# Kernel optimization log

Hardware: AMD Instinct MI355X
Metric: run time of the kernel (lower is better)

The kernel has to match this reference:

```python
import jax, jax.numpy as jnp
import numpy as np

N, E, IN_DIM, HID, OUT = 50000, 800000, 128, 64, 64


def setup_inputs() -> dict:
    key = jax.random.key(0)
    ks = jax.random.split(key, 8)
    x = jax.random.normal(ks[0], (N, IN_DIM), dtype=jnp.float32)
    edge_index = jax.random.randint(ks[1], (2, E), 0, N, dtype=jnp.int64)
    # Glorot-style init like PyG GCNConv linear; bias zeros-init equivalent -> small randn for generality
    def glorot(k, fan_in, fan_out):
        s = (6.0 / (fan_in + fan_out)) ** 0.5
        return jax.random.uniform(k, (fan_in, fan_out), jnp.float32, -s, s)
    W1 = glorot(ks[2], IN_DIM, HID)
    b1 = jnp.zeros((HID,), jnp.float32)
    W2 = glorot(ks[3], HID, HID)
    b2 = jnp.zeros((HID,), jnp.float32)
    W3 = glorot(ks[4], HID, OUT)
    b3 = jnpp = jnp.zeros((OUT,), jnp.float32)
    return {"x": x, "edge_index": edge_index, "W1": W1, "b1": b1,
            "W2": W2, "b2": b2, "W3": W3, "b3": b3}


def _gcn_norm(edge_index, num_nodes):
    # PyG gcn_norm with add_self_loops=True, edge_weight=1:
    # A_hat = A + I; deg over target column; norm = d^-1/2[src] * d^-1/2[dst]
    loops = jnp.arange(num_nodes, dtype=edge_index.dtype)
    src = jnp.concatenate([edge_index[0], loops])
    dst = jnp.concatenate([edge_index[1], loops])
    ones = jnp.ones(src.shape[0], dtype=jnp.float32)
    deg = jax.ops.segment_sum(ones, dst, num_segments=num_nodes)
    dinv = jnp.where(deg > 0, jax.lax.rsqrt(deg), 0.0)
    norm = dinv[src] * dinv[dst]  # [E+N]
    return src, dst, norm


def _conv(h, src, dst, norm, W, b, num_nodes):
    h = h @ W                         # [N, F_out] dense transform first (PyG order)
    msg = norm[:, None] * h[src]      # gather + degree-normalize, [E+N, F_out]
    out = jax.ops.segment_sum(msg, dst, num_segments=num_nodes)  # scatter-add
    return out + b


def reference(x, edge_index, W1, b1, W2, b2, W3, b3):
    num_nodes = x.shape[0]
    src, dst, norm = _gcn_norm(edge_index, num_nodes)
    h = _conv(x, src, dst, norm, W1, b1, num_nodes)
    h = jax.nn.relu(h)  # dropout is identity in eval / p=0
    h = _conv(h, src, dst, norm, W2, b2, num_nodes)
    h = jax.nn.relu(h)
    h = _conv(h, src, dst, norm, W3, b3, num_nodes)
    return h
```

## Files before the change

kernel.cpp:

```cpp
#include <hip/hip_runtime.h>


#define FD 64
#define P1CHUNK 4096

typedef unsigned short ushort_t;
typedef unsigned int uint_t;

__device__ __forceinline__ ushort_t f2bf(float f) {
    uint_t u = __float_as_uint(f);
    u = (u + 0x7fffu + ((u >> 16) & 1u)) >> 16;
    return (ushort_t)u;
}
__device__ __forceinline__ uint_t pack2bf(float f0, float f1) {
    return (uint_t)f2bf(f0) | ((uint_t)f2bf(f1) << 16);
}

__global__ __launch_bounds__(256) void bucket_count(const int* __restrict__ dst,
                                                    int* __restrict__ bucketCnt, int E) {
    __shared__ int hist[256];
    int tid = threadIdx.x;
    hist[tid] = 0;
    __syncthreads();
    int base = blockIdx.x * P1CHUNK;
#pragma unroll
    for (int k = 0; k < 16; ++k) {
        int e = base + k * 256 + tid;
        if (e < E) atomicAdd(&hist[dst[e] >> 8], 1);
    }
    __syncthreads();
    int h = hist[tid];
    if (h) atomicAdd(&bucketCnt[tid], h);
}

__global__ __launch_bounds__(256) void scan_buckets(const int* __restrict__ bucketCnt,
                                                    int* __restrict__ bucketBase,
                                                    int* __restrict__ bucketCursor,
                                                    int* __restrict__ rowptr,
                                                    int NB, int N, int E) {
    __shared__ int wsum[4];
    int tid = threadIdx.x, lane = tid & 63, wv = tid >> 6;
    int v = (tid < NB) ? bucketCnt[tid] : 0;
    int x = v;
    for (int off = 1; off < 64; off <<= 1) {
        int t = __shfl_up(x, off, 64);
        if (lane >= off) x += t;
    }
    if (lane == 63) wsum[wv] = x;
    __syncthreads();
    int wex = 0;
    for (int i = 0; i < wv; ++i) wex += wsum[i];
    int excl = wex + x - v;
    if (tid < NB) { bucketBase[tid] = excl; bucketCursor[tid] = excl; }
    if (tid == 0) { bucketBase[NB] = E; rowptr[N] = E; }
}

__global__ __launch_bounds__(256) void bin_scatter(const int* __restrict__ src,
                                                   const int* __restrict__ dst,
                                                   int* __restrict__ bucketCursor,
                                                   uint_t* __restrict__ staged, int E) {
    __shared__ int hist[256];
    __shared__ int gbase[256];
    int tid = threadIdx.x;
    hist[tid] = 0;
    __syncthreads();
    int base = blockIdx.x * P1CHUNK;
#pragma unroll
    for (int k = 0; k < 16; ++k) {
        int e = base + k * 256 + tid;
        if (e < E) atomicAdd(&hist[dst[e] >> 8], 1);
    }
    __syncthreads();
    int h = hist[tid];
    gbase[tid] = h ? atomicAdd(&bucketCursor[tid], h) : 0;
    hist[tid] = 0;
    __syncthreads();
#pragma unroll
    for (int k = 0; k < 16; ++k) {
        int e = base + k * 256 + tid;
        if (e < E) {
            int s = src[e], d = dst[e];
            int b = d >> 8;
            int r = atomicAdd(&hist[b], 1);
            staged[gbase[b] + r] = (uint_t)s | ((uint_t)(d & 255) << 16);
        }
    }
}

__global__ __launch_bounds__(256) void bucket_sort(const uint_t* __restrict__ staged,
                                                   const int* __restrict__ bucketBase,
                                                   int* __restrict__ rowptr,
                                                   float* __restrict__ dinv,
                                                   ushort_t* __restrict__ csr, int N) {
    __shared__ int ncnt[256];
    __shared__ int nrp[256];
    __shared__ int wsum[4];
    int tid = threadIdx.x, lane = tid & 63, wv = tid >> 6;
    int b = blockIdx.x;
    int gbeg = bucketBase[b], gend = bucketBase[b + 1];
    int cntE = gend - gbeg;
    ncnt[tid] = 0;
    __syncthreads();
    for (int i = tid; i < cntE; i += 256)
        atomicAdd(&ncnt[(staged[gbeg + i] >> 16) & 255], 1);
    __syncthreads();
    int v = ncnt[tid];
    int x = v;
    for (int off = 1; off < 64; off <<= 1) {
        int t = __shfl_up(x, off, 64);
        if (lane >= off) x += t;
    }
    if (lane == 63) wsum[wv] = x;
    __syncthreads();
    int wex = 0;
    for (int i = 0; i < wv; ++i) wex += wsum[i];
    int excl = wex + x - v;
    nrp[tid] = excl;
    int node = b * 256 + tid;
    if (node < N) dinv[node] = rsqrtf((float)(v + 1));
    if (node <= N) rowptr[node] = gbeg + excl;
    ncnt[tid] = 0;
    __syncthreads();
    for (int i = tid; i < cntE; i += 256) {
        uint_t p = staged[gbeg + i];
        int dl = (p >> 16) & 255;
        int lofs = atomicAdd(&ncnt[dl], 1);
        csr[(size_t)gbeg + nrp[dl] + lofs] = (ushort_t)(p & 0xffffu);
    }
}

template <int K>
__global__ __launch_bounds__(256) void gemm_kernel(const float* __restrict__ x,
                                                   const float* __restrict__ W,
                                                   const float* __restrict__ dinv,
                                                   ushort_t* __restrict__ out, int nrows) {
    constexpr int KP = K + 4;
    constexpr int NC = K / 4;
    constexpr int YP = 68;
    __shared__ float Xs[64 * KP];
    const int tid = threadIdx.x;
    const int lane = tid & 63;
    const int rowBase = blockIdx.x * 64;

    for (int idx = tid; idx < 64 * NC; idx += 256) {
        int row = idx / NC, kc = idx % NC;
        int r = rowBase + row;
        float4 v = (r < nrows) ? *(const float4*)(x + (size_t)r * K + kc * 4)
                               : make_float4(0.f, 0.f, 0.f, 0.f);
        *(float4*)(&Xs[row * KP + kc * 4]) = v;
    }
    __syncthreads();

    const int c0 = __builtin_amdgcn_readfirstlane((tid >> 6) * 16);
    float acc[16];
#pragma unroll
    for (int i = 0; i < 16; ++i) acc[i] = 0.f;
    const float* Xrow = &Xs[lane * KP];

#pragma unroll 4
    for (int k = 0; k < K; k += 4) {
        float4 xv = *(const float4*)(Xrow + k);
        const float* wp = W + (size_t)k * FD + c0;
#pragma unroll
        for (int ci = 0; ci < 16; ++ci) {
            acc[ci] = fmaf(xv.x, wp[ci], acc[ci]);
            acc[ci] = fmaf(xv.y, wp[FD + ci], acc[ci]);
            acc[ci] = fmaf(xv.z, wp[2 * FD + ci], acc[ci]);
            acc[ci] = fmaf(xv.w, wp[3 * FD + ci], acc[ci]);
        }
    }

    int r = rowBase + lane;
    float di = (r < nrows) ? dinv[r] : 0.f;
    __syncthreads();
    float* Ys = Xs;
#pragma unroll
    for (int ci = 0; ci < 16; ++ci) Ys[lane * YP + c0 + ci] = acc[ci] * di;
    __syncthreads();

    for (int i = tid; i < 64 * 16; i += 256) {
        int row = i >> 4, seg = i & 15;
        int rr = rowBase + row;
        if (rr < nrows) {
            float4 v = *(const float4*)(&Ys[row * YP + seg * 4]);
            uint2 p;
            p.x = pack2bf(v.x, v.y);
            p.y = pack2bf(v.z, v.w);
            *(uint2*)(out + (size_t)rr * FD + seg * 4) = p;
        }
    }
}

__device__ __forceinline__ void bf8_acc(uint4 a, float* acc) {
    acc[0] += __uint_as_float(a.x << 16);
    acc[1] += __uint_as_float(a.x & 0xffff0000u);
    acc[2] += __uint_as_float(a.y << 16);
    acc[3] += __uint_as_float(a.y & 0xffff0000u);
    acc[4] += __uint_as_float(a.z << 16);
    acc[5] += __uint_as_float(a.z & 0xffff0000u);
    acc[6] += __uint_as_float(a.w << 16);
    acc[7] += __uint_as_float(a.w & 0xffff0000u);
}

template <bool RELU>
__global__ __launch_bounds__(256) void agg_fused(
    const int* __restrict__ rowptr, const ushort_t* __restrict__ csr,
    const float* __restrict__ dinv, const ushort_t* __restrict__ h,
    const float* __restrict__ b, float* __restrict__ out, int N) {
    int wid = (blockIdx.x * blockDim.x + threadIdx.x) >> 6;
    int lane = threadIdx.x & 63;
    int l8 = lane & 7;
    int node = wid * 8 + (lane >> 3);
    bool valid = node < N;
    int nd = valid ? node : N - 1;
    int beg = rowptr[nd];
    int end = valid ? rowptr[nd + 1] : beg;
    const uint4* __restrict__ h4 = (const uint4*)h;
    float acc[8];
#pragma unroll
    for (int k = 0; k < 8; ++k) acc[k] = 0.f;
    bf8_acc(h4[(size_t)nd * 8 + l8], acc);
    int j = beg;
    for (; j + 3 < end; j += 4) {
        int s0 = csr[j], s1 = csr[j + 1], s2 = csr[j + 2], s3 = csr[j + 3];
        uint4 a0 = h4[(size_t)s0 * 8 + l8];
        uint4 a1 = h4[(size_t)s1 * 8 + l8];
        uint4 a2 = h4[(size_t)s2 * 8 + l8];
        uint4 a3 = h4[(size_t)s3 * 8 + l8];
        bf8_acc(a0, acc); bf8_acc(a1, acc); bf8_acc(a2, acc); bf8_acc(a3, acc);
    }
    for (; j < end; ++j) bf8_acc(h4[(size_t)csr[j] * 8 + l8], acc);

    float di = dinv[nd];
    float4 b0 = *(const float4*)(b + l8 * 8);
    float4 b1 = *(const float4*)(b + l8 * 8 + 4);
    float4 v0, v1;
    v0.x = fmaf(di, acc[0], b0.x); v0.y = fmaf(di, acc[1], b0.y);
    v0.z = fmaf(di, acc[2], b0.z); v0.w = fmaf(di, acc[3], b0.w);
    v1.x = fmaf(di, acc[4], b1.x); v1.y = fmaf(di, acc[5], b1.y);
    v1.z = fmaf(di, acc[6], b1.z); v1.w = fmaf(di, acc[7], b1.w);
    if (RELU) {
        v0.x = fmaxf(v0.x, 0.f); v0.y = fmaxf(v0.y, 0.f);
        v0.z = fmaxf(v0.z, 0.f); v0.w = fmaxf(v0.w, 0.f);
        v1.x = fmaxf(v1.x, 0.f); v1.y = fmaxf(v1.y, 0.f);
        v1.z = fmaxf(v1.z, 0.f); v1.w = fmaxf(v1.w, 0.f);
    }
    if (valid) {
        float* op = out + (size_t)node * FD + l8 * 8;
        *(float4*)op = v0;
        *(float4*)(op + 4) = v1;
    }
}

extern "C" void kernel_launch(void* const* d_in, const int* in_sizes, int n_in,
                              void* d_out, int out_size, void* d_ws, size_t ws_size,
                              hipStream_t stream) {
    const float* x  = (const float*)d_in[0];
    const int*   ei = (const int*)d_in[1];
    const float* W1 = (const float*)d_in[2];
    const float* b1 = (const float*)d_in[3];
    const float* W2 = (const float*)d_in[4];
    const float* b2 = (const float*)d_in[5];
    const float* W3 = (const float*)d_in[6];
    const float* b3 = (const float*)d_in[7];
    float* out = (float*)d_out;

    const int N = in_sizes[0] / 128;
    const int E = in_sizes[1] / 2;
    const int* src = ei;
    const int* dst = ei + E;
    const int NB = (N + 255) / 256;

    float*    f1     = (float*)d_ws;
    ushort_t* hB     = (ushort_t*)(f1 + (size_t)N * FD);
    float*    dinv   = (float*)(hB + (size_t)N * FD);
    int*      rowptr = (int*)(dinv + N);
    int*   bucketCnt    = rowptr + N + 1;
    int*   bucketBase   = bucketCnt + NB;
    int*   bucketCursor = bucketBase + NB + 1;
    uint_t*   staged = (uint_t*)(bucketCursor + NB);
    ushort_t* csr    = (ushort_t*)(staged + E);

    const int nEBlk = (E + P1CHUNK - 1) / P1CHUNK;
    dim3 blk(256);
    dim3 gGemm((N + 63) / 64);
    dim3 gAgg((N + 31) / 32);

    hipMemsetAsync(bucketCnt, 0, (size_t)NB * sizeof(int), stream);
    bucket_count<<<dim3(nEBlk), blk, 0, stream>>>(dst, bucketCnt, E);
    scan_buckets<<<dim3(1), blk, 0, stream>>>(bucketCnt, bucketBase, bucketCursor,
                                              rowptr, NB, N, E);
    bin_scatter<<<dim3(nEBlk), blk, 0, stream>>>(src, dst, bucketCursor, staged, E);
    bucket_sort<<<dim3(NB), blk, 0, stream>>>(staged, bucketBase, rowptr, dinv, csr, N);

    gemm_kernel<128><<<gGemm, blk, 0, stream>>>(x, W1, dinv, hB, N);
    agg_fused<true><<<gAgg, blk, 0, stream>>>(rowptr, csr, dinv, hB, b1, f1, N);

    gemm_kernel<64><<<gGemm, blk, 0, stream>>>(f1, W2, dinv, hB, N);
    agg_fused<true><<<gAgg, blk, 0, stream>>>(rowptr, csr, dinv, hB, b2, f1, N);

    gemm_kernel<64><<<gGemm, blk, 0, stream>>>(f1, W3, dinv, hB, N);
    agg_fused<false><<<gAgg, blk, 0, stream>>>(rowptr, csr, dinv, hB, b3, out, N);
}
```

Measured before the change: 147.7 us.

## Fuse first GEMM with edge bin scatter and defer dinv scaling to bucket sort

The layer-1 GEMM no longer depends on dinv, so it is merged into the same launch as the edge bin-scatter, with block ranges split between the two jobs. Both run concurrently and one launch is saved. The dinv row scaling of the GEMM output moves into bucket_sort, which now re-reads and rewrites hB in bf16. That adds a second bf16 rounding and an extra read-modify-write pass over hB. The combined kernel also uses the larger GEMM shared-memory footprint for the scatter blocks, which may lower their occupancy.

Result: faster. 143.1 us (-3.1%).

```diff
diff --git a/kernel.cpp b/kernel.cpp
--- a/kernel.cpp
+++ b/kernel.cpp
@@ -55,92 +55,18 @@
     if (tid == 0) { bucketBase[NB] = E; rowptr[N] = E; }
 }
 
-__global__ __launch_bounds__(256) void bin_scatter(const int* __restrict__ src,
-                                                   const int* __restrict__ dst,
-                                                   int* __restrict__ bucketCursor,
-                                                   uint_t* __restrict__ staged, int E) {
-    __shared__ int hist[256];
-    __shared__ int gbase[256];
-    int tid = threadIdx.x;
-    hist[tid] = 0;
-    __syncthreads();
-    int base = blockIdx.x * P1CHUNK;
-#pragma unroll
-    for (int k = 0; k < 16; ++k) {
-        int e = base + k * 256 + tid;
-        if (e < E) atomicAdd(&hist[dst[e] >> 8], 1);
-    }
-    __syncthreads();
-    int h = hist[tid];
-    gbase[tid] = h ? atomicAdd(&bucketCursor[tid], h) : 0;
-    hist[tid] = 0;
-    __syncthreads();
-#pragma unroll
-    for (int k = 0; k < 16; ++k) {
-        int e = base + k * 256 + tid;
-        if (e < E) {
-            int s = src[e], d = dst[e];
-            int b = d >> 8;
-            int r = atomicAdd(&hist[b], 1);
-            staged[gbase[b] + r] = (uint_t)s | ((uint_t)(d & 255) << 16);
-        }
-    }
-}
-
-__global__ __launch_bounds__(256) void bucket_sort(const uint_t* __restrict__ staged,
-                                                   const int* __restrict__ bucketBase,
-                                                   int* __restrict__ rowptr,
-                                                   float* __restrict__ dinv,
-                                                   ushort_t* __restrict__ csr, int N) {
-    __shared__ int ncnt[256];
-    __shared__ int nrp[256];
-    __shared__ int wsum[4];
-    int tid = threadIdx.x, lane = tid & 63, wv = tid >> 6;
-    int b = blockIdx.x;
-    int gbeg = bucketBase[b], gend = bucketBase[b + 1];
-    int cntE = gend - gbeg;
-    ncnt[tid] = 0;
-    __syncthreads();
-    for (int i = tid; i < cntE; i += 256)
-        atomicAdd(&ncnt[(staged[gbeg + i] >> 16) & 255], 1);
-    __syncthreads();
-    int v = ncnt[tid];
-    int x = v;
-    for (int off = 1; off < 64; off <<= 1) {
-        int t = __shfl_up(x, off, 64);
-        if (lane >= off) x += t;
-    }
-    if (lane == 63) wsum[wv] = x;
-    __syncthreads();
-    int wex = 0;
-    for (int i = 0; i < wv; ++i) wex += wsum[i];
-    int excl = wex + x - v;
-    nrp[tid] = excl;
-    int node = b * 256 + tid;
-    if (node < N) dinv[node] = rsqrtf((float)(v + 1));
-    if (node <= N) rowptr[node] = gbeg + excl;
-    ncnt[tid] = 0;
-    __syncthreads();
-    for (int i = tid; i < cntE; i += 256) {
-        uint_t p = staged[gbeg + i];
-        int dl = (p >> 16) & 255;
-        int lofs = atomicAdd(&ncnt[dl], 1);
-        csr[(size_t)gbeg + nrp[dl] + lofs] = (ushort_t)(p & 0xffffu);
-    }
-}
-
-template <int K>
-__global__ __launch_bounds__(256) void gemm_kernel(const float* __restrict__ x,
-                                                   const float* __restrict__ W,
-                                                   const float* __restrict__ dinv,
-                                                   ushort_t* __restrict__ out, int nrows) {
+template <int K, bool SCALE>
+__device__ __forceinline__ void gemm_body(int bid, const float* __restrict__ x,
+                                          const float* __restrict__ W,
+                                          const float* __restrict__ dinv,
+                                          ushort_t* __restrict__ out, int nrows,
+                                          float* Xs ) {
     constexpr int KP = K + 4;
     constexpr int NC = K / 4;
     constexpr int YP = 68;
-    __shared__ float Xs[64 * KP];
     const int tid = threadIdx.x;
     const int lane = tid & 63;
-    const int rowBase = blockIdx.x * 64;
+    const int rowBase = bid * 64;
 
     for (int idx = tid; idx < 64 * NC; idx += 256) {
         int row = idx / NC, kc = idx % NC;
@@ -171,7 +97,8 @@
     }
 
     int r = rowBase + lane;
-    float di = (r < nrows) ? dinv[r] : 0.f;
+    float di = 1.0f;
+    if (SCALE) di = (r < nrows) ? dinv[r] : 0.f;
     __syncthreads();
     float* Ys = Xs;
 #pragma unroll
@@ -187,6 +114,118 @@
             p.x = pack2bf(v.x, v.y);
             p.y = pack2bf(v.z, v.w);
             *(uint2*)(out + (size_t)rr * FD + seg * 4) = p;
+        }
+    }
+}
+
+template <int K>
+__global__ __launch_bounds__(256) void gemm_kernel(const float* __restrict__ x,
+                                                   const float* __restrict__ W,
+                                                   const float* __restrict__ dinv,
+                                                   ushort_t* __restrict__ out, int nrows) {
+    __shared__ float Xs[64 * (K + 4)];
+    gemm_body<K, true>(blockIdx.x, x, W, dinv, out, nrows, Xs);
+}
+
+__global__ __launch_bounds__(256) void fused_gemm1_scatter(
+    const float* __restrict__ x, const float* __restrict__ W1,
+    ushort_t* __restrict__ hB, int nrows,
+    const int* __restrict__ src, const int* __restrict__ dst,
+    int* __restrict__ bucketCursor, uint_t* __restrict__ staged, int E,
+    int nGemmBlk) {
+    __shared__ float Xs[64 * 132];
+    int bid = blockIdx.x;
+    if (bid < nGemmBlk) {
+        gemm_body<128, false>(bid, x, W1, nullptr, hB, nrows, Xs);
+        return;
+    }
+    int* hist = (int*)Xs;
+    int* gbase = hist + 256;
+    int tid = threadIdx.x;
+    hist[tid] = 0;
+    __syncthreads();
+    int base = (bid - nGemmBlk) * P1CHUNK;
+#pragma unroll
+    for (int k = 0; k < 16; ++k) {
+        int e = base + k * 256 + tid;
+        if (e < E) atomicAdd(&hist[dst[e] >> 8], 1);
+    }
+    __syncthreads();
+    int h = hist[tid];
+    gbase[tid] = h ? atomicAdd(&bucketCursor[tid], h) : 0;
+    hist[tid] = 0;
+    __syncthreads();
+#pragma unroll
+    for (int k = 0; k < 16; ++k) {
+        int e = base + k * 256 + tid;
+        if (e < E) {
+            int s = src[e], d = dst[e];
+            int b = d >> 8;
+            int r = atomicAdd(&hist[b], 1);
+            staged[gbase[b] + r] = (uint_t)s | ((uint_t)(d & 255) << 16);
+        }
+    }
+}
+
+__global__ __launch_bounds__(256) void bucket_sort(const uint_t* __restrict__ staged,
+                                                   const int* __restrict__ bucketBase,
+                                                   int* __restrict__ rowptr,
+                                                   float* __restrict__ dinv,
+                                                   ushort_t* __restrict__ csr,
+                                                   ushort_t* __restrict__ hB, int N) {
+    __shared__ int ncnt[256];
+    __shared__ int nrp[256];
+    __shared__ int wsum[4];
+    __shared__ float sdinv[256];
+    int tid = threadIdx.x, lane = tid & 63, wv = tid >> 6;
+    int b = blockIdx.x;
+    int gbeg = bucketBase[b], gend = bucketBase[b + 1];
+    int cntE = gend - gbeg;
+    ncnt[tid] = 0;
+    __syncthreads();
+    for (int i = tid; i < cntE; i += 256)
+        atomicAdd(&ncnt[(staged[gbeg + i] >> 16) & 255], 1);
+    __syncthreads();
+    int v = ncnt[tid];
+    int x = v;
+    for (int off = 1; off < 64; off <<= 1) {
+        int t = __shfl_up(x, off, 64);
+        if (lane >= off) x += t;
+    }
+    if (lane == 63) wsum[wv] = x;
+    __syncthreads();
+    int wex = 0;
+    for (int i = 0; i < wv; ++i) wex += wsum[i];
+    int excl = wex + x - v;
+    nrp[tid] = excl;
+    int node = b * 256 + tid;
+    float di = rsqrtf((float)(v + 1));
+    sdinv[tid] = di;
+    if (node < N) dinv[node] = di;
+    if (node <= N) rowptr[node] = gbeg + excl;
+    ncnt[tid] = 0;
+    __syncthreads();
+    for (int i = tid; i < cntE; i += 256) {
+        uint_t p = staged[gbeg + i];
+        int dl = (p >> 16) & 255;
+        int lofs = atomicAdd(&ncnt[dl], 1);
+        csr[(size_t)gbeg + nrp[dl] + lofs] = (ushort_t)(p & 0xffffu);
+    }
+    uint2* hB2 = (uint2*)hB;
+    for (int idx = tid; idx < 256 * 16; idx += 256) {
+        int row = idx >> 4, c = idx & 15;
+        int g = b * 256 + row;
+        if (g < N) {
+            float d = sdinv[row];
+            uint2 u = hB2[(size_t)g * 16 + c];
+            float f0 = __uint_as_float(u.x << 16) * d;
+            float f1 = __uint_as_float(u.x & 0xffff0000u) * d;
+            float f2 = __uint_as_float(u.y << 16) * d;
+            float f3 = __uint_as_float(u.y & 0xffff0000u) * d;
+            uint2 o;
+            o.x = pack2bf(f0, f1);
+            o.y = pack2bf(f2, f3);
+            hB2[(size_t)g * 16 + c] = o;
         }
     }
 }
@@ -281,19 +320,21 @@
     uint_t*   staged = (uint_t*)(bucketCursor + NB);
     ushort_t* csr    = (ushort_t*)(staged + E);
 
-    const int nEBlk = (E + P1CHUNK - 1) / P1CHUNK;
+    const int nSctBlk = (E + P1CHUNK - 1) / P1CHUNK;
+    const int nGemmBlk = (N + 63) / 64;
     dim3 blk(256);
-    dim3 gGemm((N + 63) / 64);
+    dim3 gGemm(nGemmBlk);
     dim3 gAgg((N + 31) / 32);
 
     hipMemsetAsync(bucketCnt, 0, (size_t)NB * sizeof(int), stream);
-    bucket_count<<<dim3(nEBlk), blk, 0, stream>>>(dst, bucketCnt, E);
+    bucket_count<<<dim3(nSctBlk), blk, 0, stream>>>(dst, bucketCnt, E);
     scan_buckets<<<dim3(1), blk, 0, stream>>>(bucketCnt, bucketBase, bucketCursor,
                                               rowptr, NB, N, E);
-    bin_scatter<<<dim3(nEBlk), blk, 0, stream>>>(src, dst, bucketCursor, staged, E);
-    bucket_sort<<<dim3(NB), blk, 0, stream>>>(staged, bucketBase, rowptr, dinv, csr, N);
-
-    gemm_kernel<128><<<gGemm, blk, 0, stream>>>(x, W1, dinv, hB, N);
+    fused_gemm1_scatter<<<dim3(nGemmBlk + nSctBlk), blk, 0, stream>>>(
+        x, W1, hB, N, src, dst, bucketCursor, staged, E, nGemmBlk);
+    bucket_sort<<<dim3(NB), blk, 0, stream>>>(staged, bucketBase, rowptr, dinv,
+                                              csr, hB, N);
+
     agg_fused<true><<<gAgg, blk, 0, stream>>>(rowptr, csr, dinv, hB, b1, f1, N);
 
     gemm_kernel<64><<<gGemm, blk, 0, stream>>>(f1, W2, dinv, hB, N);
```
